# Optimization experiments

Hardware: AMD Instinct MI355X
Metric: run time of the kernel (lower is better)

Reference implementation:

```python
import jax, jax.numpy as jnp
import numpy as np

# --- constants matching init_kwargs / defaults in the torch module ---
N_HID = 1024
N_INP = 1
DT = 0.05
RHO = 0.99
INPUT_SCALING = 1.0
GAMMA_RANGE = (2.0, 3.0)
EPS_RANGE = (0.5, 1.5)
THETA = 0.1        # spike threshold (default arg of cell)
TAU_MEM = 20.0     # LI filter time constant (default arg of forward_li_features)
FADING = False


def setup_inputs() -> dict:
    key = jax.random.key(0)
    B, T = 128, 500
    x = jax.random.normal(key, (B, T, N_INP), dtype=jnp.float32)

    rng = np.random.default_rng(0)
    # h2h = 2*(2*rand-1), then spectral_norm_scaling to spectral radius rho
    h2h = 2.0 * (2.0 * rng.random((N_HID, N_HID)) - 1.0)
    cur_rho = np.max(np.abs(np.linalg.eigvals(h2h)))
    h2h = (h2h * (RHO / cur_rho)).astype(np.float32)
    x2h = (rng.random((N_INP, N_HID)) * INPUT_SCALING).astype(np.float32)
    bias = ((rng.random(N_HID) * 2.0 - 1.0) * INPUT_SCALING).astype(np.float32)
    gamma = (rng.random(N_HID) * (GAMMA_RANGE[1] - GAMMA_RANGE[0]) + GAMMA_RANGE[0]).astype(np.float32)
    epsilon = (rng.random(N_HID) * (EPS_RANGE[1] - EPS_RANGE[0]) + EPS_RANGE[0]).astype(np.float32)

    return {
        "x": x,
        "h2h": jnp.asarray(h2h),
        "x2h": jnp.asarray(x2h),
        "bias": jnp.asarray(bias),
        "gamma": jnp.asarray(gamma),
        "epsilon": jnp.asarray(epsilon),
    }


def reference(x, h2h, x2h, bias, gamma, epsilon):
    B, T, _ = x.shape
    n_hid = h2h.shape[0]
    dt = jnp.float32(DT)
    alpha = jnp.exp(jnp.float32(-1.0 / TAU_MEM))

    def step(carry, xt):
        hy, hz, u, tot = carry
        # coupled-oscillator cell (ref_period stays identically zero in the source)
        pre = jnp.tanh(xt @ x2h + hy @ h2h + bias)       # (B, n_hid)
        hz = hz + dt * (pre - gamma * hy - epsilon * hz)
        if FADING:
            hz = hz - dt * hz
        hy = hy + dt * hz
        if FADING:
            hy = hy - dt * hy
        s = (hy - THETA > 0).astype(jnp.float32)          # spike
        u = u * alpha + s * (1.0 - alpha)                 # LI filter
        tot = tot + s.sum()
        return (hy, hz, u, tot), None

    z = jnp.zeros((B, n_hid), dtype=jnp.float32)
    init = (z, z, z, jnp.float32(0.0))
    xs = jnp.swapaxes(x, 0, 1)                            # (T, B, n_inp)
    (hy, hz, u, tot), _ = jax.lax.scan(step, init, xs)
    avg_firing_rate = tot / (B * T * n_hid)
    return u, avg_firing_rate
```

## Files before the change

kernel.cpp:

```cpp
#include <hip/hip_runtime.h>
#include <math.h>

typedef unsigned long long u64;
typedef unsigned int u32;

#define N_HID   1024
#define NBATCH  128
#define TSTEPS  500
#define DT      0.05f
#define THETA   0.1f

#define B_WG   8
#define C_WG   64
#define KSPL   8
#define KSEG   (N_HID / KSPL)
#define NGRP   (NBATCH / B_WG)
#define NCT    (N_HID / C_WG)
#define NWG    (NGRP * NCT)

#define CTRL_TOT    0
#define CTRL_GRP    64
#define CTRL_WORDS  (CTRL_GRP + NGRP * 64)

__device__ __forceinline__ u32 a_ld32(const u32* p) {
    return __hip_atomic_load(p, __ATOMIC_RELAXED, __HIP_MEMORY_SCOPE_AGENT);
}
__device__ __forceinline__ void a_st32(u32* p, u32 v) {
    __hip_atomic_store(p, v, __ATOMIC_RELAXED, __HIP_MEMORY_SCOPE_AGENT);
}
__device__ __forceinline__ u64 a_ld64(const u64* p) {
    return __hip_atomic_load(p, __ATOMIC_RELAXED, __HIP_MEMORY_SCOPE_AGENT);
}
__device__ __forceinline__ void a_st64(u64* p, u64 v) {
    __hip_atomic_store(p, v, __ATOMIC_RELAXED, __HIP_MEMORY_SCOPE_AGENT);
}

__global__ __launch_bounds__(256, 1) void persist_kernel(
    const float* __restrict__ x,
    const float* __restrict__ W,
    const float* __restrict__ x2h,
    const float* __restrict__ bias,
    const float* __restrict__ gam,
    const float* __restrict__ eps,
    float* __restrict__ hyT0,
    float* __restrict__ hyT1,
    float* __restrict__ uout,
    u32* __restrict__ ctrl,
    float alpha, float oma)
{
    __shared__ float sh_hyT[N_HID * B_WG];
    __shared__ float sh_part[KSPL * B_WG * C_WG];
    __shared__ float sh_out[C_WG * (B_WG + 1)];
    __shared__ u32 sh_cnt;

    const int tid = threadIdx.x;
    if (tid == 0) sh_cnt = 0u;

    const int bid   = blockIdx.x;
    const int xcd   = bid & 7;
    const int idx   = bid >> 3;
    const int ctile = xcd * 2 + (idx & 1);
    const int btile = idx >> 1;
    const int c0g   = ctile * C_WG;
    const int b0    = btile * B_WG;

    const int cg  = tid & 15;
    const int bg  = (tid >> 4) & 1;
    const int ks  = tid >> 5;
    const int bl0 = bg * 4;
    const int k0  = ks * KSEG;
    const float* Wp = W + (size_t)k0 * N_HID + c0g + cg * 4;

    const int wv   = tid >> 6;
    const int lane = tid & 63;
    u32* flags = ctrl + CTRL_GRP + (btile << 6);
    u32* myflag_pollp = flags + (4 * wv + (lane & 3));

    const int bl_a = tid >> 6;
    const int bl_b = 4 + bl_a;
    const int c_e  = tid & 63;
    const int cgl  = c0g + c_e;
    const float x2h_c  = x2h[cgl];
    const float bias_c = bias[cgl];
    const float gam_c  = gam[cgl];
    const float eps_c  = eps[cgl];
    const float* xrow_a = x + (size_t)(b0 + bl_a) * TSTEPS;
    const float* xrow_b = x + (size_t)(b0 + bl_b) * TSTEPS;

    float hz_a = 0.f, hz_b = 0.f, u_a = 0.f, u_b = 0.f;
    u32 spikes = 0;

    const float* src = hyT0;
    float*       dst = hyT1;

    for (int t = 0; t < TSTEPS; ++t) {
        if (t == 0) {
            u64* s64 = (u64*)sh_hyT;
            #pragma unroll
            for (int it = 0; it < 16; ++it) s64[it * 256 + tid] = 0ull;
            __syncthreads();
        } else {
            while (!__all(a_ld32(myflag_pollp) >= (u32)t))
                __builtin_amdgcn_s_sleep(1);
            u64 tmp[16];
            #pragma unroll
            for (int it = 0; it < 16; ++it) {
                const int i    = it * 64 + lane;
                const int k    = (wv << 8) + (i >> 2);
                const int pair = i & 3;
                const u64* sp = (const u64*)(src + (size_t)k * NBATCH + b0) + pair;
                tmp[it] = a_ld64(sp);
            }
            u64* s64 = (u64*)sh_hyT;
            #pragma unroll
            for (int it = 0; it < 16; ++it)
                s64[(wv << 10) + it * 64 + lane] = tmp[it];
        }

        float acc[4][4];
        #pragma unroll
        for (int i = 0; i < 4; ++i)
            #pragma unroll
            for (int jj = 0; jj < 4; ++jj) acc[i][jj] = 0.f;

        #pragma unroll 8
        for (int kk = 0; kk < KSEG; ++kk) {
            const float4 hv = *(const float4*)(&sh_hyT[(k0 + kk) * B_WG + bl0]);
            const float4 wv4 = *(const float4*)(Wp + (size_t)kk * N_HID);
            acc[0][0] = fmaf(hv.x, wv4.x, acc[0][0]);
            acc[0][1] = fmaf(hv.x, wv4.y, acc[0][1]);
            acc[0][2] = fmaf(hv.x, wv4.z, acc[0][2]);
            acc[0][3] = fmaf(hv.x, wv4.w, acc[0][3]);
            acc[1][0] = fmaf(hv.y, wv4.x, acc[1][0]);
            acc[1][1] = fmaf(hv.y, wv4.y, acc[1][1]);
            acc[1][2] = fmaf(hv.y, wv4.z, acc[1][2]);
            acc[1][3] = fmaf(hv.y, wv4.w, acc[1][3]);
            acc[2][0] = fmaf(hv.z, wv4.x, acc[2][0]);
            acc[2][1] = fmaf(hv.z, wv4.y, acc[2][1]);
            acc[2][2] = fmaf(hv.z, wv4.z, acc[2][2]);
            acc[2][3] = fmaf(hv.z, wv4.w, acc[2][3]);
            acc[3][0] = fmaf(hv.w, wv4.x, acc[3][0]);
            acc[3][1] = fmaf(hv.w, wv4.y, acc[3][1]);
            acc[3][2] = fmaf(hv.w, wv4.z, acc[3][2]);
            acc[3][3] = fmaf(hv.w, wv4.w, acc[3][3]);
        }

        #pragma unroll
        for (int bi = 0; bi < 4; ++bi) {
            float4 v = make_float4(acc[bi][0], acc[bi][1], acc[bi][2], acc[bi][3]);
            *(float4*)(&sh_part[((ks * B_WG) + bl0 + bi) * C_WG + cg * 4]) = v;
        }
        __syncthreads();

        {
            float sum = sh_part[(0 * B_WG + bl_a) * C_WG + c_e];
            #pragma unroll
            for (int s2 = 1; s2 < KSPL; ++s2)
                sum += sh_part[(s2 * B_WG + bl_a) * C_WG + c_e];
            const float xb  = xrow_a[t];
            const float pre = tanhf(fmaf(xb, x2h_c, sum) + bias_c);
            const float hyv = sh_hyT[cgl * B_WG + bl_a];
            hz_a = fmaf(DT, pre - gam_c * hyv - eps_c * hz_a, hz_a);
            const float hyn = fmaf(DT, hz_a, hyv);
            const int s = ((hyn - THETA) > 0.f) ? 1 : 0;
            u_a = fmaf(u_a, alpha, (float)s * oma);
            spikes += (u32)s;
            sh_out[c_e * (B_WG + 1) + bl_a] = hyn;
        }
        {
            float sum = sh_part[(0 * B_WG + bl_b) * C_WG + c_e];
            #pragma unroll
            for (int s2 = 1; s2 < KSPL; ++s2)
                sum += sh_part[(s2 * B_WG + bl_b) * C_WG + c_e];
            const float xb  = xrow_b[t];
            const float pre = tanhf(fmaf(xb, x2h_c, sum) + bias_c);
            const float hyv = sh_hyT[cgl * B_WG + bl_b];
            hz_b = fmaf(DT, pre - gam_c * hyv - eps_c * hz_b, hz_b);
            const float hyn = fmaf(DT, hz_b, hyv);
            const int s = ((hyn - THETA) > 0.f) ? 1 : 0;
            u_b = fmaf(u_b, alpha, (float)s * oma);
            spikes += (u32)s;
            sh_out[c_e * (B_WG + 1) + bl_b] = hyn;
        }
        __syncthreads();

        {
            const int c2 = tid >> 3;
            #pragma unroll
            for (int rr = 0; rr < 2; ++rr) {
                const int c3 = c2 + rr * 32;
                const int b2 = (tid & 7);
                (void)c3; (void)b2;
            }
        }
        {
            const int c2 = tid >> 2;
            const int b2 = (tid & 3) * 2;
            float2 f2 = make_float2(sh_out[c2 * (B_WG + 1) + b2],
                                    sh_out[c2 * (B_WG + 1) + b2 + 1]);
            u64 v;
            __builtin_memcpy(&v, &f2, 8);
            a_st64((u64*)(dst + (size_t)(c0g + c2) * NBATCH + b0 + b2), v);
        }
        __syncthreads();

        if (tid == 0) a_st32(flags + ctile, (u32)(t + 1));

        float* tmpp = (float*)src; src = dst; dst = tmpp;
    }

    uout[(size_t)(b0 + bl_a) * N_HID + cgl] = u_a;
    uout[(size_t)(b0 + bl_b) * N_HID + cgl] = u_b;

    u32 s = spikes;
    s += __shfl_down(s, 32);
    s += __shfl_down(s, 16);
    s += __shfl_down(s, 8);
    s += __shfl_down(s, 4);
    s += __shfl_down(s, 2);
    s += __shfl_down(s, 1);
    if ((tid & 63) == 0) atomicAdd(&sh_cnt, s);
    __syncthreads();
    if (tid == 0) atomicAdd(ctrl + CTRL_TOT, sh_cnt);
}

__global__ void init_kernel(u32* ctrl)
{
    const int i = blockIdx.x * blockDim.x + threadIdx.x;
    if (i < CTRL_WORDS) {
        __hip_atomic_store(ctrl + i, 0u, __ATOMIC_RELAXED,
                           __HIP_MEMORY_SCOPE_AGENT);
    }
}

__global__ void final_kernel(const u32* __restrict__ ctrl,
                             float* __restrict__ out_rate)
{
    if (threadIdx.x == 0 && blockIdx.x == 0) {
        const double denom = (double)NBATCH * (double)TSTEPS * (double)N_HID;
        *out_rate = (float)((double)ctrl[CTRL_TOT] / denom);
    }
}

extern "C" void kernel_launch(void* const* d_in, const int* in_sizes, int n_in,
                              void* d_out, int out_size, void* d_ws, size_t ws_size,
                              hipStream_t stream)
{
    const float* x    = (const float*)d_in[0];
    const float* h2h  = (const float*)d_in[1];
    const float* x2h  = (const float*)d_in[2];
    const float* bias = (const float*)d_in[3];
    const float* gam  = (const float*)d_in[4];
    const float* eps  = (const float*)d_in[5];

    float* out = (float*)d_out;

    float* hyT0 = (float*)d_ws;
    float* hyT1 = hyT0 + (size_t)NBATCH * N_HID;
    u32*   ctrl = (u32*)(hyT1 + (size_t)NBATCH * N_HID);

    init_kernel<<<dim3((CTRL_WORDS + 255) / 256), dim3(256), 0, stream>>>(ctrl);

    float alpha = expf(-1.0f / 20.0f);
    float oma   = 1.0f - alpha;

    void* args[] = {
        (void*)&x, (void*)&h2h, (void*)&x2h, (void*)&bias, (void*)&gam,
        (void*)&eps, (void*)&hyT0, (void*)&hyT1, (void*)&out, (void*)&ctrl,
        (void*)&alpha, (void*)&oma
    };
    hipLaunchCooperativeKernel((const void*)persist_kernel,
                               dim3(NWG), dim3(256), args, 0, stream);

    final_kernel<<<dim3(1), dim3(64), 0, stream>>>(
        ctrl, out + (size_t)NBATCH * N_HID);
}
```

Measured before the change: 3.665 ms.

## Replace group flags with epoch-tagged hidden-state values and overlap loads with FMA

Each hidden-state element is now written to global memory as a 64-bit word: the float value plus the step number as an epoch tag. Readers spin on the individual words instead of on per-tile flags, which removes the flag store, the staging of outputs through shared memory and two block barriers per step. The shared hidden-state and partial-sum buffers are double-buffered so the trailing barrier can go. The second half of the state load is issued before the first half of the matrix-vector work, so fetch latency overlaps compute. In exchange, global state traffic doubles and correctness depends on stale epoch tags never matching the expected step.

```diff
diff --git a/kernel.cpp b/kernel.cpp
--- a/kernel.cpp
+++ b/kernel.cpp
@@ -19,15 +19,8 @@
 #define NWG    (NGRP * NCT)
 
 #define CTRL_TOT    0
-#define CTRL_GRP    64
-#define CTRL_WORDS  (CTRL_GRP + NGRP * 64)
-
-__device__ __forceinline__ u32 a_ld32(const u32* p) {
-    return __hip_atomic_load(p, __ATOMIC_RELAXED, __HIP_MEMORY_SCOPE_AGENT);
-}
-__device__ __forceinline__ void a_st32(u32* p, u32 v) {
-    __hip_atomic_store(p, v, __ATOMIC_RELAXED, __HIP_MEMORY_SCOPE_AGENT);
-}
+#define CTRL_WORDS  64
+
 __device__ __forceinline__ u64 a_ld64(const u64* p) {
     return __hip_atomic_load(p, __ATOMIC_RELAXED, __HIP_MEMORY_SCOPE_AGENT);
 }
@@ -42,15 +35,14 @@
     const float* __restrict__ bias,
     const float* __restrict__ gam,
     const float* __restrict__ eps,
-    float* __restrict__ hyT0,
-    float* __restrict__ hyT1,
+    u64* __restrict__ hyA,
+    u64* __restrict__ hyB,
     float* __restrict__ uout,
     u32* __restrict__ ctrl,
     float alpha, float oma)
 {
-    __shared__ float sh_hyT[N_HID * B_WG];
-    __shared__ float sh_part[KSPL * B_WG * C_WG];
-    __shared__ float sh_out[C_WG * (B_WG + 1)];
+    __shared__ float sh_hyT[2][N_HID * B_WG / 1];
+    __shared__ float sh_part[2][KSPL * B_WG * C_WG];
     __shared__ u32 sh_cnt;
 
     const int tid = threadIdx.x;
@@ -73,8 +65,6 @@
 
     const int wv   = tid >> 6;
     const int lane = tid & 63;
-    u32* flags = ctrl + CTRL_GRP + (btile << 6);
-    u32* myflag_pollp = flags + (4 * wv + (lane & 3));
 
     const int bl_a = tid >> 6;
     const int bl_b = 4 + bl_a;
@@ -90,32 +80,14 @@
     float hz_a = 0.f, hz_b = 0.f, u_a = 0.f, u_b = 0.f;
     u32 spikes = 0;
 
-    const float* src = hyT0;
-    float*       dst = hyT1;
-
     for (int t = 0; t < TSTEPS; ++t) {
-        if (t == 0) {
-            u64* s64 = (u64*)sh_hyT;
-            #pragma unroll
-            for (int it = 0; it < 16; ++it) s64[it * 256 + tid] = 0ull;
-            __syncthreads();
-        } else {
-            while (!__all(a_ld32(myflag_pollp) >= (u32)t))
-                __builtin_amdgcn_s_sleep(1);
-            u64 tmp[16];
-            #pragma unroll
-            for (int it = 0; it < 16; ++it) {
-                const int i    = it * 64 + lane;
-                const int k    = (wv << 8) + (i >> 2);
-                const int pair = i & 3;
-                const u64* sp = (const u64*)(src + (size_t)k * NBATCH + b0) + pair;
-                tmp[it] = a_ld64(sp);
-            }
-            u64* s64 = (u64*)sh_hyT;
-            #pragma unroll
-            for (int it = 0; it < 16; ++it)
-                s64[(wv << 10) + it * 64 + lane] = tmp[it];
-        }
+        const u64* srcU = (t & 1) ? hyB : hyA;
+        u64*       dstU = (t & 1) ? hyA : hyB;
+        float* hyt  = sh_hyT[t & 1];
+        float* part = sh_part[t & 1];
+
+        const float xa = xrow_a[t];
+        const float xb = xrow_b[t];
 
         float acc[4][4];
         #pragma unroll
@@ -123,90 +95,121 @@
             #pragma unroll
             for (int jj = 0; jj < 4; ++jj) acc[i][jj] = 0.f;
 
-        #pragma unroll 8
-        for (int kk = 0; kk < KSEG; ++kk) {
-            const float4 hv = *(const float4*)(&sh_hyT[(k0 + kk) * B_WG + bl0]);
-            const float4 wv4 = *(const float4*)(Wp + (size_t)kk * N_HID);
-            acc[0][0] = fmaf(hv.x, wv4.x, acc[0][0]);
-            acc[0][1] = fmaf(hv.x, wv4.y, acc[0][1]);
-            acc[0][2] = fmaf(hv.x, wv4.z, acc[0][2]);
-            acc[0][3] = fmaf(hv.x, wv4.w, acc[0][3]);
-            acc[1][0] = fmaf(hv.y, wv4.x, acc[1][0]);
-            acc[1][1] = fmaf(hv.y, wv4.y, acc[1][1]);
-            acc[1][2] = fmaf(hv.y, wv4.z, acc[1][2]);
-            acc[1][3] = fmaf(hv.y, wv4.w, acc[1][3]);
-            acc[2][0] = fmaf(hv.z, wv4.x, acc[2][0]);
-            acc[2][1] = fmaf(hv.z, wv4.y, acc[2][1]);
-            acc[2][2] = fmaf(hv.z, wv4.z, acc[2][2]);
-            acc[2][3] = fmaf(hv.z, wv4.w, acc[2][3]);
-            acc[3][0] = fmaf(hv.w, wv4.x, acc[3][0]);
-            acc[3][1] = fmaf(hv.w, wv4.y, acc[3][1]);
-            acc[3][2] = fmaf(hv.w, wv4.z, acc[3][2]);
-            acc[3][3] = fmaf(hv.w, wv4.w, acc[3][3]);
+        auto fma_half = [&](int kbeg) {
+            #pragma unroll 8
+            for (int kk2 = 0; kk2 < 64; ++kk2) {
+                const int kk = kbeg + kk2;
+                const float4 hv  = *(const float4*)(&hyt[(k0 + kk) * B_WG + bl0]);
+                const float4 wv4 = *(const float4*)(Wp + (size_t)kk * N_HID);
+                acc[0][0] = fmaf(hv.x, wv4.x, acc[0][0]);
+                acc[0][1] = fmaf(hv.x, wv4.y, acc[0][1]);
+                acc[0][2] = fmaf(hv.x, wv4.z, acc[0][2]);
+                acc[0][3] = fmaf(hv.x, wv4.w, acc[0][3]);
+                acc[1][0] = fmaf(hv.y, wv4.x, acc[1][0]);
+                acc[1][1] = fmaf(hv.y, wv4.y, acc[1][1]);
+                acc[1][2] = fmaf(hv.y, wv4.z, acc[1][2]);
+                acc[1][3] = fmaf(hv.y, wv4.w, acc[1][3]);
+                acc[2][0] = fmaf(hv.z, wv4.x, acc[2][0]);
+                acc[2][1] = fmaf(hv.z, wv4.y, acc[2][1]);
+                acc[2][2] = fmaf(hv.z, wv4.z, acc[2][2]);
+                acc[2][3] = fmaf(hv.z, wv4.w, acc[2][3]);
+                acc[3][0] = fmaf(hv.w, wv4.x, acc[3][0]);
+                acc[3][1] = fmaf(hv.w, wv4.y, acc[3][1]);
+                acc[3][2] = fmaf(hv.w, wv4.z, acc[3][2]);
+                acc[3][3] = fmaf(hv.w, wv4.w, acc[3][3]);
+            }
+        };
+
+        if (t == 0) {
+            u64* s64 = (u64*)hyt;
+            #pragma unroll
+            for (int it = 0; it < 16; ++it)
+                s64[(wv << 10) + it * 64 + lane] = 0ull;
+            fma_half(0);
+            fma_half(64);
+        } else {
+            const u32 ep = (u32)t;
+            u64 ta[16];
+            #pragma unroll
+            for (int i = 0; i < 16; ++i) {
+                const int it = (i < 8) ? i : (i + 8);
+                const int e  = it * 64 + lane;
+                const int k  = (wv << 8) + (e >> 3);
+                ta[i] = a_ld64(srcU + (size_t)k * NBATCH + b0 + (e & 7));
+            }
+            #pragma unroll
+            for (int i = 0; i < 16; ++i) {
+                const int it = (i < 8) ? i : (i + 8);
+                const int e  = it * 64 + lane;
+                const int k  = (wv << 8) + (e >> 3);
+                u64 v = ta[i];
+                while ((u32)(v >> 32) != ep) {
+                    __builtin_amdgcn_s_sleep(1);
+                    v = a_ld64(srcU + (size_t)k * NBATCH + b0 + (e & 7));
+                }
+                hyt[k * B_WG + (e & 7)] = __uint_as_float((u32)v);
+            }
+            u64 tb[16];
+            #pragma unroll
+            for (int i = 0; i < 16; ++i) {
+                const int it = (i < 8) ? (i + 8) : (i + 16);
+                const int e  = it * 64 + lane;
+                const int k  = (wv << 8) + (e >> 3);
+                tb[i] = a_ld64(srcU + (size_t)k * NBATCH + b0 + (e & 7));
+            }
+            fma_half(0);
+            #pragma unroll
+            for (int i = 0; i < 16; ++i) {
+                const int it = (i < 8) ? (i + 8) : (i + 16);
+                const int e  = it * 64 + lane;
+                const int k  = (wv << 8) + (e >> 3);
+                u64 v = tb[i];
+                while ((u32)(v >> 32) != ep) {
+                    __builtin_amdgcn_s_sleep(1);
+                    v = a_ld64(srcU + (size_t)k * NBATCH + b0 + (e & 7));
+                }
+                hyt[k * B_WG + (e & 7)] = __uint_as_float((u32)v);
+            }
+            fma_half(64);
         }
 
         #pragma unroll
         for (int bi = 0; bi < 4; ++bi) {
             float4 v = make_float4(acc[bi][0], acc[bi][1], acc[bi][2], acc[bi][3]);
-            *(float4*)(&sh_part[((ks * B_WG) + bl0 + bi) * C_WG + cg * 4]) = v;
+            *(float4*)(&part[((ks * B_WG) + bl0 + bi) * C_WG + cg * 4]) = v;
         }
         __syncthreads();
 
         {
-            float sum = sh_part[(0 * B_WG + bl_a) * C_WG + c_e];
+            float sum = part[(0 * B_WG + bl_a) * C_WG + c_e];
             #pragma unroll
             for (int s2 = 1; s2 < KSPL; ++s2)
-                sum += sh_part[(s2 * B_WG + bl_a) * C_WG + c_e];
-            const float xb  = xrow_a[t];
-            const float pre = tanhf(fmaf(xb, x2h_c, sum) + bias_c);
-            const float hyv = sh_hyT[cgl * B_WG + bl_a];
+                sum += part[(s2 * B_WG + bl_a) * C_WG + c_e];
+            const float pre = tanhf(fmaf(xa, x2h_c, sum) + bias_c);
+            const float hyv = hyt[cgl * B_WG + bl_a];
             hz_a = fmaf(DT, pre - gam_c * hyv - eps_c * hz_a, hz_a);
             const float hyn = fmaf(DT, hz_a, hyv);
             const int s = ((hyn - THETA) > 0.f) ? 1 : 0;
             u_a = fmaf(u_a, alpha, (float)s * oma);
             spikes += (u32)s;
-            sh_out[c_e * (B_WG + 1) + bl_a] = hyn;
+            const u64 pv = ((u64)(u32)(t + 1) << 32) | (u64)__float_as_uint(hyn);
+            a_st64(dstU + (size_t)cgl * NBATCH + b0 + bl_a, pv);
         }
         {
-            float sum = sh_part[(0 * B_WG + bl_b) * C_WG + c_e];
+            float sum = part[(0 * B_WG + bl_b) * C_WG + c_e];
             #pragma unroll
             for (int s2 = 1; s2 < KSPL; ++s2)
-                sum += sh_part[(s2 * B_WG + bl_b) * C_WG + c_e];
-            const float xb  = xrow_b[t];
+                sum += part[(s2 * B_WG + bl_b) * C_WG + c_e];
             const float pre = tanhf(fmaf(xb, x2h_c, sum) + bias_c);
-            const float hyv = sh_hyT[cgl * B_WG + bl_b];
+            const float hyv = hyt[cgl * B_WG + bl_b];
             hz_b = fmaf(DT, pre - gam_c * hyv - eps_c * hz_b, hz_b);
             const float hyn = fmaf(DT, hz_b, hyv);
             const int s = ((hyn - THETA) > 0.f) ? 1 : 0;
             u_b = fmaf(u_b, alpha, (float)s * oma);
             spikes += (u32)s;
-            sh_out[c_e * (B_WG + 1) + bl_b] = hyn;
-        }
-        __syncthreads();
-
-        {
-            const int c2 = tid >> 3;
-            #pragma unroll
-            for (int rr = 0; rr < 2; ++rr) {
-                const int c3 = c2 + rr * 32;
-                const int b2 = (tid & 7);
-                (void)c3; (void)b2;
-            }
-        }
-        {
-            const int c2 = tid >> 2;
-            const int b2 = (tid & 3) * 2;
-            float2 f2 = make_float2(sh_out[c2 * (B_WG + 1) + b2],
-                                    sh_out[c2 * (B_WG + 1) + b2 + 1]);
-            u64 v;
-            __builtin_memcpy(&v, &f2, 8);
-            a_st64((u64*)(dst + (size_t)(c0g + c2) * NBATCH + b0 + b2), v);
-        }
-        __syncthreads();
-
-        if (tid == 0) a_st32(flags + ctile, (u32)(t + 1));
-
-        float* tmpp = (float*)src; src = dst; dst = tmpp;
+            const u64 pv = ((u64)(u32)(t + 1) << 32) | (u64)__float_as_uint(hyn);
+            a_st64(dstU + (size_t)cgl * NBATCH + b0 + bl_b, pv);
+        }
     }
 
     uout[(size_t)(b0 + bl_a) * N_HID + cgl] = u_a;
@@ -255,18 +258,18 @@
 
     float* out = (float*)d_out;
 
-    float* hyT0 = (float*)d_ws;
-    float* hyT1 = hyT0 + (size_t)NBATCH * N_HID;
-    u32*   ctrl = (u32*)(hyT1 + (size_t)NBATCH * N_HID);
-
-    init_kernel<<<dim3((CTRL_WORDS + 255) / 256), dim3(256), 0, stream>>>(ctrl);
+    u64* hyA  = (u64*)d_ws;
+    u64* hyB  = hyA + (size_t)N_HID * NBATCH;
+    u32* ctrl = (u32*)(hyB + (size_t)N_HID * NBATCH);
+
+    init_kernel<<<dim3(1), dim3(256), 0, stream>>>(ctrl);
 
     float alpha = expf(-1.0f / 20.0f);
     float oma   = 1.0f - alpha;
 
     void* args[] = {
         (void*)&x, (void*)&h2h, (void*)&x2h, (void*)&bias, (void*)&gam,
-        (void*)&eps, (void*)&hyT0, (void*)&hyT1, (void*)&out, (void*)&ctrl,
+        (void*)&eps, (void*)&hyA, (void*)&hyB, (void*)&out, (void*)&ctrl,
         (void*)&alpha, (void*)&oma
     };
     hipLaunchCooperativeKernel((const void*)persist_kernel,
```

After: 9.566 ms. 161% more time.

## Double-buffer LDS and publish per-wave flags to drop per-step barriers

Applied to the files above, without the earlier changes.

Shared hy and partial-sum buffers are double-buffered by step parity, and the gather-through-shared-memory output stage is removed in favour of each thread storing its own hy values directly to global memory. Each wave now publishes its own readiness flag after waiting for its stores, and consumers poll 64 per-wave flags instead of 16 per-tile flags. This removes two of the three __syncthreads per timestep and the staging step, at the cost of scattered 4-byte stores instead of 8-byte ones, more flag traffic, and reliance on a relaxed waitcnt for store visibility ordering.

```diff
diff --git a/kernel.cpp b/kernel.cpp
--- a/kernel.cpp
+++ b/kernel.cpp
@@ -31,9 +31,17 @@
 __device__ __forceinline__ u64 a_ld64(const u64* p) {
     return __hip_atomic_load(p, __ATOMIC_RELAXED, __HIP_MEMORY_SCOPE_AGENT);
 }
-__device__ __forceinline__ void a_st64(u64* p, u64 v) {
-    __hip_atomic_store(p, v, __ATOMIC_RELAXED, __HIP_MEMORY_SCOPE_AGENT);
-}
+
+#define FMA16(hv, wv4) do { \
+    acc[0][0]=fmaf((hv).x,(wv4).x,acc[0][0]); acc[0][1]=fmaf((hv).x,(wv4).y,acc[0][1]); \
+    acc[0][2]=fmaf((hv).x,(wv4).z,acc[0][2]); acc[0][3]=fmaf((hv).x,(wv4).w,acc[0][3]); \
+    acc[1][0]=fmaf((hv).y,(wv4).x,acc[1][0]); acc[1][1]=fmaf((hv).y,(wv4).y,acc[1][1]); \
+    acc[1][2]=fmaf((hv).y,(wv4).z,acc[1][2]); acc[1][3]=fmaf((hv).y,(wv4).w,acc[1][3]); \
+    acc[2][0]=fmaf((hv).z,(wv4).x,acc[2][0]); acc[2][1]=fmaf((hv).z,(wv4).y,acc[2][1]); \
+    acc[2][2]=fmaf((hv).z,(wv4).z,acc[2][2]); acc[2][3]=fmaf((hv).z,(wv4).w,acc[2][3]); \
+    acc[3][0]=fmaf((hv).w,(wv4).x,acc[3][0]); acc[3][1]=fmaf((hv).w,(wv4).y,acc[3][1]); \
+    acc[3][2]=fmaf((hv).w,(wv4).z,acc[3][2]); acc[3][3]=fmaf((hv).w,(wv4).w,acc[3][3]); \
+} while (0)
 
 __global__ __launch_bounds__(256, 1) void persist_kernel(
     const float* __restrict__ x,
@@ -48,9 +56,8 @@
     u32* __restrict__ ctrl,
     float alpha, float oma)
 {
-    __shared__ float sh_hyT[N_HID * B_WG];
-    __shared__ float sh_part[KSPL * B_WG * C_WG];
-    __shared__ float sh_out[C_WG * (B_WG + 1)];
+    __shared__ float sh_hyT[2][N_HID * B_WG];
+    __shared__ float sh_part[2][KSPL * B_WG * C_WG];
     __shared__ u32 sh_cnt;
 
     const int tid = threadIdx.x;
@@ -74,7 +81,8 @@
     const int wv   = tid >> 6;
     const int lane = tid & 63;
     u32* flags = ctrl + CTRL_GRP + (btile << 6);
-    u32* myflag_pollp = flags + (4 * wv + (lane & 3));
+    u32* mypoll  = flags + 16 * wv + (lane & 15);
+    u32* mypub   = flags + ctile * 4 + wv;
 
     const int bl_a = tid >> 6;
     const int bl_b = 4 + bl_a;
@@ -90,17 +98,22 @@
     float hz_a = 0.f, hz_b = 0.f, u_a = 0.f, u_b = 0.f;
     u32 spikes = 0;
 
-    const float* src = hyT0;
-    float*       dst = hyT1;
-
     for (int t = 0; t < TSTEPS; ++t) {
+        const float* src = (t & 1) ? hyT1 : hyT0;
+        float*       dst = (t & 1) ? hyT0 : hyT1;
+        float* hyt  = sh_hyT[t & 1];
+        float* part = sh_part[t & 1];
+
+        const float xa = xrow_a[t];
+        const float xb = xrow_b[t];
+
         if (t == 0) {
-            u64* s64 = (u64*)sh_hyT;
-            #pragma unroll
-            for (int it = 0; it < 16; ++it) s64[it * 256 + tid] = 0ull;
-            __syncthreads();
+            u64* s64 = (u64*)hyt;
+            #pragma unroll
+            for (int it = 0; it < 16; ++it)
+                s64[(wv << 10) + it * 64 + lane] = 0ull;
         } else {
-            while (!__all(a_ld32(myflag_pollp) >= (u32)t))
+            while (!__all(a_ld32(mypoll) >= (u32)t))
                 __builtin_amdgcn_s_sleep(1);
             u64 tmp[16];
             #pragma unroll
@@ -111,7 +124,7 @@
                 const u64* sp = (const u64*)(src + (size_t)k * NBATCH + b0) + pair;
                 tmp[it] = a_ld64(sp);
             }
-            u64* s64 = (u64*)sh_hyT;
+            u64* s64 = (u64*)hyt;
             #pragma unroll
             for (int it = 0; it < 16; ++it)
                 s64[(wv << 10) + it * 64 + lane] = tmp[it];
@@ -125,88 +138,51 @@
 
         #pragma unroll 8
         for (int kk = 0; kk < KSEG; ++kk) {
-            const float4 hv = *(const float4*)(&sh_hyT[(k0 + kk) * B_WG + bl0]);
+            const float4 hv  = *(const float4*)(&hyt[(k0 + kk) * B_WG + bl0]);
             const float4 wv4 = *(const float4*)(Wp + (size_t)kk * N_HID);
-            acc[0][0] = fmaf(hv.x, wv4.x, acc[0][0]);
-            acc[0][1] = fmaf(hv.x, wv4.y, acc[0][1]);
-            acc[0][2] = fmaf(hv.x, wv4.z, acc[0][2]);
-            acc[0][3] = fmaf(hv.x, wv4.w, acc[0][3]);
-            acc[1][0] = fmaf(hv.y, wv4.x, acc[1][0]);
-            acc[1][1] = fmaf(hv.y, wv4.y, acc[1][1]);
-            acc[1][2] = fmaf(hv.y, wv4.z, acc[1][2]);
-            acc[1][3] = fmaf(hv.y, wv4.w, acc[1][3]);
-            acc[2][0] = fmaf(hv.z, wv4.x, acc[2][0]);
-            acc[2][1] = fmaf(hv.z, wv4.y, acc[2][1]);
-            acc[2][2] = fmaf(hv.z, wv4.z, acc[2][2]);
-            acc[2][3] = fmaf(hv.z, wv4.w, acc[2][3]);
-            acc[3][0] = fmaf(hv.w, wv4.x, acc[3][0]);
-            acc[3][1] = fmaf(hv.w, wv4.y, acc[3][1]);
-            acc[3][2] = fmaf(hv.w, wv4.z, acc[3][2]);
-            acc[3][3] = fmaf(hv.w, wv4.w, acc[3][3]);
+            FMA16(hv, wv4);
         }
 
         #pragma unroll
         for (int bi = 0; bi < 4; ++bi) {
             float4 v = make_float4(acc[bi][0], acc[bi][1], acc[bi][2], acc[bi][3]);
-            *(float4*)(&sh_part[((ks * B_WG) + bl0 + bi) * C_WG + cg * 4]) = v;
+            *(float4*)(&part[((ks * B_WG) + bl0 + bi) * C_WG + cg * 4]) = v;
         }
         __syncthreads();
 
         {
-            float sum = sh_part[(0 * B_WG + bl_a) * C_WG + c_e];
+            float sum = part[(0 * B_WG + bl_a) * C_WG + c_e];
             #pragma unroll
             for (int s2 = 1; s2 < KSPL; ++s2)
-                sum += sh_part[(s2 * B_WG + bl_a) * C_WG + c_e];
-            const float xb  = xrow_a[t];
-            const float pre = tanhf(fmaf(xb, x2h_c, sum) + bias_c);
-            const float hyv = sh_hyT[cgl * B_WG + bl_a];
+                sum += part[(s2 * B_WG + bl_a) * C_WG + c_e];
+            const float pre = tanhf(fmaf(xa, x2h_c, sum) + bias_c);
+            const float hyv = hyt[cgl * B_WG + bl_a];
             hz_a = fmaf(DT, pre - gam_c * hyv - eps_c * hz_a, hz_a);
             const float hyn = fmaf(DT, hz_a, hyv);
             const int s = ((hyn - THETA) > 0.f) ? 1 : 0;
             u_a = fmaf(u_a, alpha, (float)s * oma);
             spikes += (u32)s;
-            sh_out[c_e * (B_WG + 1) + bl_a] = hyn;
+            a_st32((u32*)(dst + (size_t)cgl * NBATCH + b0 + bl_a),
+                   __float_as_uint(hyn));
         }
         {
-            float sum = sh_part[(0 * B_WG + bl_b) * C_WG + c_e];
+            float sum = part[(0 * B_WG + bl_b) * C_WG + c_e];
             #pragma unroll
             for (int s2 = 1; s2 < KSPL; ++s2)
-                sum += sh_part[(s2 * B_WG + bl_b) * C_WG + c_e];
-            const float xb  = xrow_b[t];
+                sum += part[(s2 * B_WG + bl_b) * C_WG + c_e];
             const float pre = tanhf(fmaf(xb, x2h_c, sum) + bias_c);
-            const float hyv = sh_hyT[cgl * B_WG + bl_b];
+            const float hyv = hyt[cgl * B_WG + bl_b];
             hz_b = fmaf(DT, pre - gam_c * hyv - eps_c * hz_b, hz_b);
             const float hyn = fmaf(DT, hz_b, hyv);
             const int s = ((hyn - THETA) > 0.f) ? 1 : 0;
             u_b = fmaf(u_b, alpha, (float)s * oma);
             spikes += (u32)s;
-            sh_out[c_e * (B_WG + 1) + bl_b] = hyn;
-        }
-        __syncthreads();
-
-        {
-            const int c2 = tid >> 3;
-            #pragma unroll
-            for (int rr = 0; rr < 2; ++rr) {
-                const int c3 = c2 + rr * 32;
-                const int b2 = (tid & 7);
-                (void)c3; (void)b2;
-            }
-        }
-        {
-            const int c2 = tid >> 2;
-            const int b2 = (tid & 3) * 2;
-            float2 f2 = make_float2(sh_out[c2 * (B_WG + 1) + b2],
-                                    sh_out[c2 * (B_WG + 1) + b2 + 1]);
-            u64 v;
-            __builtin_memcpy(&v, &f2, 8);
-            a_st64((u64*)(dst + (size_t)(c0g + c2) * NBATCH + b0 + b2), v);
-        }
-        __syncthreads();
-
-        if (tid == 0) a_st32(flags + ctile, (u32)(t + 1));
-
-        float* tmpp = (float*)src; src = dst; dst = tmpp;
+            a_st32((u32*)(dst + (size_t)cgl * NBATCH + b0 + bl_b),
+                   __float_as_uint(hyn));
+        }
+
+        asm volatile("s_waitcnt vmcnt(0)" ::: "memory");
+        if (lane == 0) a_st32(mypub, (u32)(t + 1));
     }
 
     uout[(size_t)(b0 + bl_a) * N_HID + cgl] = u_a;
```

After: 4.808 ms. 1.31x slower.
